# Performance work log

Measured on AMD Instinct MI355X. Metric: run time of the kernel, lower is better.

Reference implementation:

```python
import jax, jax.numpy as jnp
import numpy as np

DIM = 180
HEADS = 6
NSQ = 12          # num_gs_seed_sqrt
N = NSQ * NSQ     # 144 tokens per window
B = 2048


def _relative_position_index(nsq: int) -> np.ndarray:
    coords = np.stack(np.meshgrid(np.arange(nsq), np.arange(nsq), indexing='ij'))  # [2,nsq,nsq]
    flat = coords.reshape(2, -1)                       # [2, N]
    rel = flat[:, :, None] - flat[:, None, :]          # [2, N, N]
    rel = rel.transpose(1, 2, 0)                       # [N, N, 2]
    rel[:, :, 0] += nsq - 1
    rel[:, :, 1] += nsq - 1
    rel[:, :, 0] *= 2 * nsq - 1
    return rel.sum(-1)                                 # [N, N] int

REL_IDX = jnp.asarray(_relative_position_index(NSQ))


def setup_inputs() -> dict:
    key = jax.random.key(0)
    ks = jax.random.split(key, 10)
    d = DIM
    std_lin = 1.0 / np.sqrt(d)
    inp = {
        'gs': jax.random.normal(ks[0], (B, N, d), dtype=jnp.float32),
        'wq': jax.random.normal(ks[1], (d, d), dtype=jnp.float32) * std_lin,
        'bq': jnp.zeros((d,), jnp.float32),
        'wk': jax.random.normal(ks[2], (d, d), dtype=jnp.float32) * std_lin,
        'bk': jnp.zeros((d,), jnp.float32),
        'wv': jax.random.normal(ks[3], (d, d), dtype=jnp.float32) * std_lin,
        'bv': jnp.zeros((d,), jnp.float32),
        'wp': jax.random.normal(ks[4], (d, d), dtype=jnp.float32) * std_lin,
        'bp': jnp.zeros((d,), jnp.float32),
        # trunc_normal(std=0.02) table: [(2*nsq-1)^2, heads]
        'bias_table': jax.random.normal(ks[5], ((2 * NSQ - 1) ** 2, HEADS), dtype=jnp.float32) * 0.02,
    }
    return inp


def reference(gs, wq, bq, wk, bk, wv, bv, wp, bp, bias_table):
    b, n, c = gs.shape
    h = HEADS
    hd = c // h
    scale = hd ** -0.5

    def heads(x, w, bias):
        y = x @ w + bias                                  # [b, n, c]
        return y.reshape(b, n, h, hd).transpose(0, 2, 1, 3)  # [b, h, n, hd]

    q = heads(gs, wq, bq) * scale
    k = heads(gs, wk, bk)
    v = heads(gs, wv, bv)

    attn = jnp.einsum('bhqd,bhkd->bhqk', q, k)            # [b, h, n, n]
    rel_bias = bias_table[REL_IDX]                        # [n, n, h]
    attn = attn + rel_bias.transpose(2, 0, 1)[None]       # + [1, h, n, n]
    attn = jax.nn.softmax(attn, axis=-1)

    out = jnp.einsum('bhqk,bhkd->bhqd', attn, v)          # [b, h, n, hd]
    out = out.transpose(0, 2, 1, 3).reshape(b, n, c)
    return out @ wp + bp
```

## Files before the change

### kernel.cpp

```cpp
#include <hip/hip_runtime.h>


typedef __bf16 bf16_t;
typedef __bf16 bf16x8 __attribute__((ext_vector_type(8)));
typedef __bf16 bf16x4 __attribute__((ext_vector_type(4)));
typedef float f32x4 __attribute__((ext_vector_type(4)));

#define MFMA16(a, b, c) __builtin_amdgcn_mfma_f32_16x16x32_bf16((a), (b), (c), 0, 0, 0)
#define GLDS16(g, l) __builtin_amdgcn_global_load_lds(                         \
    (const __attribute__((address_space(1))) void*)(g),                        \
    (__attribute__((address_space(3))) void*)(l), 16, 0, 0)

static __device__ __forceinline__ f32x4 fzero4() {
    f32x4 z; z[0] = 0.f; z[1] = 0.f; z[2] = 0.f; z[3] = 0.f; return z;
}
static __device__ __forceinline__ bf16x8 bzero8() {
    bf16x8 z;
    #pragma unroll
    for (int i = 0; i < 8; ++i) z[i] = (bf16_t)0.f;
    return z;
}

__global__ void pack_kernel(const float* __restrict__ wq, const float* __restrict__ bq,
                            const float* __restrict__ wk, const float* __restrict__ bk,
                            const float* __restrict__ wv, const float* __restrict__ bv,
                            const float* __restrict__ wp, const float* __restrict__ bt,
                            bf16_t* __restrict__ Wqkv, bf16_t* __restrict__ Wp,
                            bf16_t* __restrict__ BIASf, float* __restrict__ bqkv)
{
    const int t = blockIdx.x * blockDim.x + threadIdx.x;
    const int stride = gridDim.x * blockDim.x;
    const float L2E = 1.4426950408889634f;
    const float qscale = 0.18257418583505536f * L2E;

    for (int i = t; i < 6 * 6 * 6 * 512; i += stride) {
        int j = i & 7, lane = (i >> 3) & 63;
        int f = i >> 9;
        int nt = f % 6, kt = (f / 6) % 6, h = f / 36;
        int kin = kt * 32 + (lane >> 4) * 8 + j;
        int c = nt * 16 + (lane & 15);
        int sec = c >> 5, d = c & 31;
        float v = 0.f;
        if (kin < 180 && d < 30) {
            int col = h * 30 + d;
            if (sec == 0)      v = wq[kin * 180 + col] * qscale;
            else if (sec == 1) v = wk[kin * 180 + col];
            else               v = wv[kin * 180 + col];
        }
        Wqkv[i] = (bf16_t)v;
    }
    for (int i = t; i < 2 * 6 * 6 * 512; i += stride) {
        int j = i & 7, lane = (i >> 3) & 63;
        int f = i >> 9;
        int ntl = f % 6, kt = (f / 6) % 6, half = f / 36;
        int nt = half * 6 + ntl;
        int kin = kt * 32 + (lane >> 4) * 8 + j;
        int hh = kin >> 5, d = kin & 31;
        int cout = nt * 16 + (lane & 15);
        float v = 0.f;
        if (d < 30 && cout < 180) v = wp[(hh * 30 + d) * 180 + cout];
        Wp[i] = (bf16_t)v;
    }
    for (int i = t; i < 6 * 9 * 9 * 64; i += stride) {
        int lane = i & 63;
        int f = i >> 6;
        int nt = f % 9, wvq = (f / 9) % 9, h = f / 81;
        int q = wvq * 16 + (lane & 15);
        int qi = q / 12, qj = q % 12;
        #pragma unroll
        for (int r = 0; r < 4; ++r) {
            int k = nt * 16 + (lane >> 4) * 4 + r;
            int ki = k / 12, kj = k % 12;
            int rel = (qi - ki + 11) * 23 + (qj - kj + 11);
            BIASf[i * 4 + r] = (bf16_t)(bt[rel * 6 + h] * L2E);
        }
    }
    for (int i = t; i < 576; i += stride) {
        int c = i % 96, h = i / 96;
        int sec = c >> 5, d = c & 31;
        float v = 0.f;
        if (d < 30) {
            if (sec == 0)      v = bq[h * 30 + d] * qscale;
            else if (sec == 1) v = bk[h * 30 + d];
            else               v = bv[h * 30 + d];
        }
        bqkv[i] = v;
    }
}

__global__ __launch_bounds__(576, 2)
void attn_kernel(const float* __restrict__ gs,
                 const bf16_t* __restrict__ Wqkv, const bf16_t* __restrict__ Wp,
                 const bf16_t* __restrict__ BIASf, const float* __restrict__ bqkv,
                 const float* __restrict__ bp, float* __restrict__ out)
{
    __shared__ __align__(16) unsigned char smem[152064];

    const int tid = threadIdx.x;
    const int lane = tid & 63;
    const int wv = tid >> 6;
    const int l15 = lane & 15;
    const int lg = lane >> 4;
    const int win = blockIdx.x;
    const float* __restrict__ gsw = gs + (size_t)win * 25920;

    constexpr int WB0     = 0;
    constexpr int WB1     = 36864;
    constexpr int ST_BASE = 73728;
    constexpr int K_BASE  = 115200;
    constexpr int VT_BASE = 133632;

    #pragma unroll
    for (int i = 0; i < 4; ++i) {
        const int base = wv * 64 + i * 576;
        GLDS16((const char*)Wqkv + (size_t)(base + lane) * 16, smem + WB0 + base * 16);
    }
    #pragma unroll
    for (int i = 0; i < 4; ++i) {
        const int base = wv * 64 + i * 576;
        GLDS16((const char*)Wqkv + 36864 + (size_t)(base + lane) * 16, smem + WB1 + base * 16);
    }

    bf16x8 xa[6];
    {
        const int row = wv * 16 + l15;
        const float4* __restrict__ g4 = (const float4*)(gsw + row * 180);
        #pragma unroll
        for (int kt = 0; kt < 6; ++kt) {
            const int c0 = kt * 32 + lg * 8;
            float4 lo = {0.f, 0.f, 0.f, 0.f}, hi = {0.f, 0.f, 0.f, 0.f};
            if (c0 + 4 <= 180) lo = g4[c0 >> 2];
            if (c0 + 8 <= 180) hi = g4[(c0 >> 2) + 1];
            bf16x8 v;
            v[0] = (bf16_t)lo.x; v[1] = (bf16_t)lo.y; v[2] = (bf16_t)lo.z; v[3] = (bf16_t)lo.w;
            v[4] = (bf16_t)hi.x; v[5] = (bf16_t)hi.y; v[6] = (bf16_t)hi.z; v[7] = (bf16_t)hi.w;
            xa[kt] = v;
        }
    }
    __syncthreads();

    bf16x8 ao[6];
    char* const pb = (char*)smem + ST_BASE + wv * 4608;
    const int pswz = (l15 & 6) << 3;
    const int row0 = wv * 16 + lg * 4;

    auto qkv_scatter = [&](const int hh, const int wbofs, bf16_t* q8o) {
        const int KB = K_BASE + (hh & 1) * 9216;
        const int VB = VT_BASE + (hh & 1) * 9216;
        f32x4 acc[6];
        #pragma unroll
        for (int nt = 0; nt < 6; ++nt) acc[nt] = fzero4();
        __builtin_amdgcn_s_setprio(1);
        #pragma unroll
        for (int kt = 0; kt < 6; ++kt) {
            #pragma unroll
            for (int nt = 0; nt < 6; ++nt) {
                bf16x8 bw = *(const bf16x8*)(smem + wbofs + ((kt * 6 + nt) * 64 + lane) * 16);
                acc[nt] = MFMA16(xa[kt], bw, acc[nt]);
            }
        }
        __builtin_amdgcn_s_setprio(0);
        #pragma unroll
        for (int nt = 0; nt < 2; ++nt) {
            const float bias = bqkv[hh * 96 + nt * 16 + l15];
            #pragma unroll
            for (int r = 0; r < 4; ++r)
                q8o[nt * 4 + r] = (bf16_t)(acc[nt][r] + bias);
        }
        #pragma unroll
        for (int nt = 2; nt < 4; ++nt) {
            const float bias = bqkv[hh * 96 + nt * 16 + l15];
            const int d32 = ((nt & 1) << 4) + l15;
            #pragma unroll
            for (int r = 0; r < 4; ++r) {
                const int rr = row0 + r;
                *(bf16_t*)(smem + KB + rr * 64 + ((d32 * 2) ^ ((rr & 6) << 3))) =
                    (bf16_t)(acc[nt][r] + bias);
            }
        }
        #pragma unroll
        for (int nt = 4; nt < 6; ++nt) {
            const float bias = bqkv[hh * 96 + nt * 16 + l15];
            const int d32 = ((nt & 1) << 4) + l15;
            const int vswz = (wv < 8) ? (((d32 >> 2) & 3) << 4) : 0;
            bf16x4 vvv;
            #pragma unroll
            for (int r = 0; r < 4; ++r)
                vvv[r] = (bf16_t)(acc[nt][r] + bias);
            *(bf16x4*)(smem + VB + d32 * 288 + ((row0 * 2) ^ vswz)) = vvv;
        }
    };

    #pragma unroll
    for (int i3 = 0; i3 < 3; ++i3) {
        const int h0 = i3 * 2, h1 = h0 + 1;

        bf16_t q8a[8], q8b[8];
        qkv_scatter(h0, WB0, q8a);
        qkv_scatter(h1, WB1, q8b);
        __syncthreads();

        {
            const char* __restrict__ n0 = (i3 < 2)
                ? ((const char*)Wqkv + (size_t)(h0 + 2) * 36864) : (const char*)Wp;
            const char* __restrict__ n1 = (i3 < 2)
                ? ((const char*)Wqkv + (size_t)(h1 + 2) * 36864) : ((const char*)Wp + 36864);
            #pragma unroll
            for (int i = 0; i < 4; ++i) {
                const int base = wv * 64 + i * 576;
                GLDS16(n0 + (size_t)(base + lane) * 16, smem + WB0 + base * 16);
            }
            #pragma unroll
            for (int i = 0; i < 4; ++i) {
                const int base = wv * 64 + i * 576;
                GLDS16(n1 + (size_t)(base + lane) * 16, smem + WB1 + base * 16);
            }
        }

        #pragma unroll
        for (int r = 0; r < 4; ++r) {
            const int row = lg * 4 + r;
            const int swz = (row & 6) << 3;
            *(bf16_t*)(pb + row * 64 + ((l15 * 2) ^ swz))             = q8a[r];
            *(bf16_t*)(pb + row * 64 + ((l15 * 2 + 32) ^ swz))        = q8a[4 + r];
            *(bf16_t*)(pb + 1024 + row * 64 + ((l15 * 2) ^ swz))      = q8b[r];
            *(bf16_t*)(pb + 1024 + row * 64 + ((l15 * 2 + 32) ^ swz)) = q8b[4 + r];
        }
        asm volatile("" ::: "memory");
        bf16x8 aq0 = *(const bf16x8*)(pb + l15 * 64 + ((lg * 16) ^ ((l15 & 6) << 3)));
        bf16x8 aq1 = *(const bf16x8*)(pb + 1024 + l15 * 64 + ((lg * 16) ^ ((l15 & 6) << 3)));
        asm volatile("" ::: "memory");

        float sum0 = 0.f, sum1 = 0.f;
        f32x4 s1[9];
        #pragma unroll
        for (int nt = 0; nt < 9; ++nt) {
            const int krow = nt * 16 + l15;
            const int ksw = (lg * 16) ^ ((krow & 6) << 3);
            bf16x8 kf0 = *(const bf16x8*)(smem + K_BASE + krow * 64 + ksw);
            bf16x8 kf1 = *(const bf16x8*)(smem + K_BASE + 9216 + krow * 64 + ksw);
            f32x4 sv0 = MFMA16(kf0, aq0, fzero4());
            f32x4 sv1 = MFMA16(kf1, aq1, fzero4());
            bf16x4 b40 = *(const bf16x4*)(BIASf +
                         (size_t)((((h0 * 9 + wv) * 9 + nt) * 64 + lane) * 4));
            bf16x4 b41 = *(const bf16x4*)(BIASf +
                         (size_t)((((h1 * 9 + wv) * 9 + nt) * 64 + lane) * 4));
            bf16x4 pw;
            #pragma unroll
            for (int r = 0; r < 4; ++r) {
                float p = exp2f(sv0[r] + (float)b40[r]);
                sum0 += p;
                pw[r] = (bf16_t)p;
                float q = exp2f(sv1[r] + (float)b41[r]);
                sum1 += q;
                s1[nt][r] = q;
            }
            if (nt < 8)
                *(bf16x4*)(pb + (nt >> 1) * 1024 + l15 * 64 +
                           ((((nt & 1) << 5) + lg * 8) ^ pswz)) = pw;
            else
                *(bf16x4*)(pb + 4096 + l15 * 32 + lg * 8) = pw;
        }
        sum0 += __shfl_xor(sum0, 16, 64);
        sum0 += __shfl_xor(sum0, 32, 64);
        sum1 += __shfl_xor(sum1, 16, 64);
        sum1 += __shfl_xor(sum1, 32, 64);
        const float rinv0 = 1.f / sum0;
        const float rinv1 = 1.f / sum1;
        asm volatile("" ::: "memory");

        f32x4 o00 = fzero4(), o01 = fzero4();
        __builtin_amdgcn_s_setprio(1);
        #pragma unroll
        for (int kt = 0; kt < 4; ++kt) {
            const int vs0 = ((l15 >> 2) & 3) << 4;
            bf16x8 ap  = *(const bf16x8*)(pb + kt * 1024 + l15 * 64 + ((lg * 16) ^ pswz));
            bf16x8 bv0 = *(const bf16x8*)(smem + VT_BASE + l15 * 288 + kt * 64 + ((lg * 16) ^ vs0));
            bf16x8 bv1 = *(const bf16x8*)(smem + VT_BASE + (16 + l15) * 288 + kt * 64 + ((lg * 16) ^ vs0));
            o00 = MFMA16(ap, bv0, o00);
            o01 = MFMA16(ap, bv1, o01);
        }
        {
            bf16x8 ap = bzero8(), bv0 = bzero8(), bv1 = bzero8();
            if (lg < 2) {
                ap  = *(const bf16x8*)(pb + 4096 + l15 * 32 + lg * 16);
                bv0 = *(const bf16x8*)(smem + VT_BASE + l15 * 288 + 256 + lg * 16);
                bv1 = *(const bf16x8*)(smem + VT_BASE + (16 + l15) * 288 + 256 + lg * 16);
            }
            o00 = MFMA16(ap, bv0, o00);
            o01 = MFMA16(ap, bv1, o01);
        }
        __builtin_amdgcn_s_setprio(0);
        asm volatile("" ::: "memory");

        #pragma unroll
        for (int nt = 0; nt < 9; ++nt) {
            bf16x4 pw;
            #pragma unroll
            for (int r = 0; r < 4; ++r) pw[r] = (bf16_t)s1[nt][r];
            if (nt < 8)
                *(bf16x4*)(pb + (nt >> 1) * 1024 + l15 * 64 +
                           ((((nt & 1) << 5) + lg * 8) ^ pswz)) = pw;
            else
                *(bf16x4*)(pb + 4096 + l15 * 32 + lg * 8) = pw;
        }
        asm volatile("" ::: "memory");

        f32x4 o10 = fzero4(), o11 = fzero4();
        __builtin_amdgcn_s_setprio(1);
        #pragma unroll
        for (int kt = 0; kt < 4; ++kt) {
            const int vs0 = ((l15 >> 2) & 3) << 4;
            bf16x8 ap  = *(const bf16x8*)(pb + kt * 1024 + l15 * 64 + ((lg * 16) ^ pswz));
            bf16x8 bv0 = *(const bf16x8*)(smem + VT_BASE + 9216 + l15 * 288 + kt * 64 + ((lg * 16) ^ vs0));
            bf16x8 bv1 = *(const bf16x8*)(smem + VT_BASE + 9216 + (16 + l15) * 288 + kt * 64 + ((lg * 16) ^ vs0));
            o10 = MFMA16(ap, bv0, o10);
            o11 = MFMA16(ap, bv1, o11);
        }
        {
            bf16x8 ap = bzero8(), bv0 = bzero8(), bv1 = bzero8();
            if (lg < 2) {
                ap  = *(const bf16x8*)(pb + 4096 + l15 * 32 + lg * 16);
                bv0 = *(const bf16x8*)(smem + VT_BASE + 9216 + l15 * 288 + 256 + lg * 16);
                bv1 = *(const bf16x8*)(smem + VT_BASE + 9216 + (16 + l15) * 288 + 256 + lg * 16);
            }
            o10 = MFMA16(ap, bv0, o10);
            o11 = MFMA16(ap, bv1, o11);
        }
        __builtin_amdgcn_s_setprio(0);
        asm volatile("" ::: "memory");

        #pragma unroll
        for (int r = 0; r < 4; ++r) {
            const float rq0 = __shfl(rinv0, lg * 4 + r, 16);
            const float rq1 = __shfl(rinv1, lg * 4 + r, 16);
            const int row = lg * 4 + r;
            const int swz = (row & 6) << 3;
            *(bf16_t*)(pb + row * 64 + ((l15 * 2) ^ swz))             = (bf16_t)(o00[r] * rq0);
            *(bf16_t*)(pb + row * 64 + ((l15 * 2 + 32) ^ swz))        = (bf16_t)(o01[r] * rq0);
            *(bf16_t*)(pb + 1024 + row * 64 + ((l15 * 2) ^ swz))      = (bf16_t)(o10[r] * rq1);
            *(bf16_t*)(pb + 1024 + row * 64 + ((l15 * 2 + 32) ^ swz)) = (bf16_t)(o11[r] * rq1);
        }
        asm volatile("" ::: "memory");
        ao[h0] = *(const bf16x8*)(pb + l15 * 64 + ((lg * 16) ^ ((l15 & 6) << 3)));
        ao[h1] = *(const bf16x8*)(pb + 1024 + l15 * 64 + ((lg * 16) ^ ((l15 & 6) << 3)));

        __syncthreads();
    }

    float* __restrict__ og = out + (size_t)win * 25920;
    #pragma unroll
    for (int half = 0; half < 2; ++half) {
        const int WH = half ? WB1 : WB0;
        f32x4 accp[6];
        #pragma unroll
        for (int nt = 0; nt < 6; ++nt) accp[nt] = fzero4();
        __builtin_amdgcn_s_setprio(1);
        #pragma unroll
        for (int kt = 0; kt < 6; ++kt) {
            #pragma unroll
            for (int nt = 0; nt < 6; ++nt) {
                bf16x8 bw = *(const bf16x8*)(smem + WH + ((kt * 6 + nt) * 64 + lane) * 16);
                accp[nt] = MFMA16(ao[kt], bw, accp[nt]);
            }
        }
        __builtin_amdgcn_s_setprio(0);
        #pragma unroll
        for (int nt = 0; nt < 6; ++nt) {
            const int col = half * 96 + nt * 16 + l15;
            if (col < 180) {
                const float bias = bp[col];
                #pragma unroll
                for (int r = 0; r < 4; ++r) {
                    const int row = wv * 16 + lg * 4 + r;
                    og[row * 180 + col] = accp[nt][r] + bias;
                }
            }
        }
    }
}

extern "C" void kernel_launch(void* const* d_in, const int* in_sizes, int n_in,
                              void* d_out, int out_size, void* d_ws, size_t ws_size,
                              hipStream_t stream) {
    const float* gs = (const float*)d_in[0];
    const float* wq = (const float*)d_in[1];
    const float* bq = (const float*)d_in[2];
    const float* wk = (const float*)d_in[3];
    const float* bk = (const float*)d_in[4];
    const float* wv = (const float*)d_in[5];
    const float* bv = (const float*)d_in[6];
    const float* wp = (const float*)d_in[7];
    const float* bp = (const float*)d_in[8];
    const float* bt = (const float*)d_in[9];

    char* ws = (char*)d_ws;
    bf16_t* Wqkv  = (bf16_t*)(ws);
    bf16_t* Wp    = (bf16_t*)(ws + 221184);
    bf16_t* BIASf = (bf16_t*)(ws + 294912);
    float*  bqkv  = (float*)(ws + 543744);

    pack_kernel<<<256, 256, 0, stream>>>(wq, bq, wk, bk, wv, bv, wp, bt,
                                         Wqkv, Wp, BIASf, bqkv);
    attn_kernel<<<2048, 576, 0, stream>>>(gs, Wqkv, Wp, BIASf, bqkv, bp, (float*)d_out);
}
```

Measured before the change: 325.2 us.

## Feed softmax probabilities directly into 16x16x16 MFMA, skipping LDS staging

The P·V product now uses the K=16 bf16 MFMA so the exp'd score registers can serve directly as the A operand, removing the round trip of P through per-wave LDS scratch and the second pass that stored head1's probabilities. Both heads' PV accumulation is interleaved into the score loop, and the scratch region shrinks, cutting LDS allocation per block. This trades twice as many smaller MFMAs and narrower V loads for fewer LDS writes and reads. An inline-asm fallback with s_nop padding is used if the builtin is missing.

```diff
diff --git a/kernel.cpp b/kernel.cpp
--- a/kernel.cpp
+++ b/kernel.cpp
@@ -4,6 +4,7 @@
 typedef __bf16 bf16_t;
 typedef __bf16 bf16x8 __attribute__((ext_vector_type(8)));
 typedef __bf16 bf16x4 __attribute__((ext_vector_type(4)));
+typedef short s16x4 __attribute__((ext_vector_type(4)));
 typedef float f32x4 __attribute__((ext_vector_type(4)));
 
 #define MFMA16(a, b, c) __builtin_amdgcn_mfma_f32_16x16x32_bf16((a), (b), (c), 0, 0, 0)
@@ -11,14 +12,25 @@
     (const __attribute__((address_space(1))) void*)(g),                        \
     (__attribute__((address_space(3))) void*)(l), 16, 0, 0)
 
+static __device__ __forceinline__ s16x4 b2s(bf16x4 v) {
+    s16x4 r; __builtin_memcpy(&r, &v, 8); return r;
+}
+#if __has_builtin(__builtin_amdgcn_mfma_f32_16x16x16bf16_1k)
+static __device__ __forceinline__ f32x4 mfma_k16(bf16x4 a, bf16x4 b, f32x4 c) {
+    return __builtin_amdgcn_mfma_f32_16x16x16bf16_1k(b2s(a), b2s(b), c, 0, 0, 0);
+}
+#define K16_ASM 0
+#else
+static __device__ __forceinline__ f32x4 mfma_k16(bf16x4 a, bf16x4 b, f32x4 c) {
+    asm volatile("v_mfma_f32_16x16x16_bf16 %0, %1, %2, %0"
+                 : "+v"(c) : "v"(a), "v"(b));
+    return c;
+}
+#define K16_ASM 1
+#endif
+
 static __device__ __forceinline__ f32x4 fzero4() {
     f32x4 z; z[0] = 0.f; z[1] = 0.f; z[2] = 0.f; z[3] = 0.f; return z;
-}
-static __device__ __forceinline__ bf16x8 bzero8() {
-    bf16x8 z;
-    #pragma unroll
-    for (int i = 0; i < 8; ++i) z[i] = (bf16_t)0.f;
-    return z;
 }
 
 __global__ void pack_kernel(const float* __restrict__ wq, const float* __restrict__ bq,
@@ -94,7 +106,7 @@
                  const bf16_t* __restrict__ BIASf, const float* __restrict__ bqkv,
                  const float* __restrict__ bp, float* __restrict__ out)
 {
-    __shared__ __align__(16) unsigned char smem[152064];
+    __shared__ __align__(16) unsigned char smem[129024];
 
     const int tid = threadIdx.x;
     const int lane = tid & 63;
@@ -107,8 +119,8 @@
     constexpr int WB0     = 0;
     constexpr int WB1     = 36864;
     constexpr int ST_BASE = 73728;
-    constexpr int K_BASE  = 115200;
-    constexpr int VT_BASE = 133632;
+    constexpr int K_BASE  = 92160;
+    constexpr int VT_BASE = 110592;
 
     #pragma unroll
     for (int i = 0; i < 4; ++i) {
@@ -140,8 +152,7 @@
     __syncthreads();
 
     bf16x8 ao[6];
-    char* const pb = (char*)smem + ST_BASE + wv * 4608;
-    const int pswz = (l15 & 6) << 3;
+    char* const pb = (char*)smem + ST_BASE + wv * 2048;
     const int row0 = wv * 16 + lg * 4;
 
     auto qkv_scatter = [&](const int hh, const int wbofs, bf16_t* q8o) {
@@ -232,7 +243,7 @@
         asm volatile("" ::: "memory");
 
         float sum0 = 0.f, sum1 = 0.f;
-        f32x4 s1[9];
+        f32x4 o00 = fzero4(), o01 = fzero4(), o10 = fzero4(), o11 = fzero4();
         #pragma unroll
         for (int nt = 0; nt < 9; ++nt) {
             const int krow = nt * 16 + l15;
@@ -245,91 +256,38 @@
                          (size_t)((((h0 * 9 + wv) * 9 + nt) * 64 + lane) * 4));
             bf16x4 b41 = *(const bf16x4*)(BIASf +
                          (size_t)((((h1 * 9 + wv) * 9 + nt) * 64 + lane) * 4));
-            bf16x4 pw;
+            bf16x4 p0, p1;
             #pragma unroll
             for (int r = 0; r < 4; ++r) {
-                float p = exp2f(sv0[r] + (float)b40[r]);
-                sum0 += p;
-                pw[r] = (bf16_t)p;
-                float q = exp2f(sv1[r] + (float)b41[r]);
-                sum1 += q;
-                s1[nt][r] = q;
-            }
-            if (nt < 8)
-                *(bf16x4*)(pb + (nt >> 1) * 1024 + l15 * 64 +
-                           ((((nt & 1) << 5) + lg * 8) ^ pswz)) = pw;
-            else
-                *(bf16x4*)(pb + 4096 + l15 * 32 + lg * 8) = pw;
-        }
+                float e0 = exp2f(sv0[r] + (float)b40[r]);
+                sum0 += e0;
+                p0[r] = (bf16_t)e0;
+                float e1 = exp2f(sv1[r] + (float)b41[r]);
+                sum1 += e1;
+                p1[r] = (bf16_t)e1;
+            }
+            const int vtoff = nt * 32 + lg * 8;
+            const int vsw = (nt < 8) ? (((l15 >> 2) & 3) << 4) : 0;
+            bf16x4 v00 = *(const bf16x4*)(smem + VT_BASE + l15 * 288 + (vtoff ^ vsw));
+            bf16x4 v01 = *(const bf16x4*)(smem + VT_BASE + (16 + l15) * 288 + (vtoff ^ vsw));
+            bf16x4 v10 = *(const bf16x4*)(smem + VT_BASE + 9216 + l15 * 288 + (vtoff ^ vsw));
+            bf16x4 v11 = *(const bf16x4*)(smem + VT_BASE + 9216 + (16 + l15) * 288 + (vtoff ^ vsw));
+            o00 = mfma_k16(p0, v00, o00);
+            o01 = mfma_k16(p0, v01, o01);
+            o10 = mfma_k16(p1, v10, o10);
+            o11 = mfma_k16(p1, v11, o11);
+        }
+#if K16_ASM
+        asm volatile("s_nop 7\n\ts_nop 7");
+#endif
         sum0 += __shfl_xor(sum0, 16, 64);
         sum0 += __shfl_xor(sum0, 32, 64);
         sum1 += __shfl_xor(sum1, 16, 64);
         sum1 += __shfl_xor(sum1, 32, 64);
         const float rinv0 = 1.f / sum0;
         const float rinv1 = 1.f / sum1;
+
         asm volatile("" ::: "memory");
-
-        f32x4 o00 = fzero4(), o01 = fzero4();
-        __builtin_amdgcn_s_setprio(1);
-        #pragma unroll
-        for (int kt = 0; kt < 4; ++kt) {
-            const int vs0 = ((l15 >> 2) & 3) << 4;
-            bf16x8 ap  = *(const bf16x8*)(pb + kt * 1024 + l15 * 64 + ((lg * 16) ^ pswz));
-            bf16x8 bv0 = *(const bf16x8*)(smem + VT_BASE + l15 * 288 + kt * 64 + ((lg * 16) ^ vs0));
-            bf16x8 bv1 = *(const bf16x8*)(smem + VT_BASE + (16 + l15) * 288 + kt * 64 + ((lg * 16) ^ vs0));
-            o00 = MFMA16(ap, bv0, o00);
-            o01 = MFMA16(ap, bv1, o01);
-        }
-        {
-            bf16x8 ap = bzero8(), bv0 = bzero8(), bv1 = bzero8();
-            if (lg < 2) {
-                ap  = *(const bf16x8*)(pb + 4096 + l15 * 32 + lg * 16);
-                bv0 = *(const bf16x8*)(smem + VT_BASE + l15 * 288 + 256 + lg * 16);
-                bv1 = *(const bf16x8*)(smem + VT_BASE + (16 + l15) * 288 + 256 + lg * 16);
-            }
-            o00 = MFMA16(ap, bv0, o00);
-            o01 = MFMA16(ap, bv1, o01);
-        }
-        __builtin_amdgcn_s_setprio(0);
-        asm volatile("" ::: "memory");
-
-        #pragma unroll
-        for (int nt = 0; nt < 9; ++nt) {
-            bf16x4 pw;
-            #pragma unroll
-            for (int r = 0; r < 4; ++r) pw[r] = (bf16_t)s1[nt][r];
-            if (nt < 8)
-                *(bf16x4*)(pb + (nt >> 1) * 1024 + l15 * 64 +
-                           ((((nt & 1) << 5) + lg * 8) ^ pswz)) = pw;
-            else
-                *(bf16x4*)(pb + 4096 + l15 * 32 + lg * 8) = pw;
-        }
-        asm volatile("" ::: "memory");
-
-        f32x4 o10 = fzero4(), o11 = fzero4();
-        __builtin_amdgcn_s_setprio(1);
-        #pragma unroll
-        for (int kt = 0; kt < 4; ++kt) {
-            const int vs0 = ((l15 >> 2) & 3) << 4;
-            bf16x8 ap  = *(const bf16x8*)(pb + kt * 1024 + l15 * 64 + ((lg * 16) ^ pswz));
-            bf16x8 bv0 = *(const bf16x8*)(smem + VT_BASE + 9216 + l15 * 288 + kt * 64 + ((lg * 16) ^ vs0));
-            bf16x8 bv1 = *(const bf16x8*)(smem + VT_BASE + 9216 + (16 + l15) * 288 + kt * 64 + ((lg * 16) ^ vs0));
-            o10 = MFMA16(ap, bv0, o10);
-            o11 = MFMA16(ap, bv1, o11);
-        }
-        {
-            bf16x8 ap = bzero8(), bv0 = bzero8(), bv1 = bzero8();
-            if (lg < 2) {
-                ap  = *(const bf16x8*)(pb + 4096 + l15 * 32 + lg * 16);
-                bv0 = *(const bf16x8*)(smem + VT_BASE + 9216 + l15 * 288 + 256 + lg * 16);
-                bv1 = *(const bf16x8*)(smem + VT_BASE + 9216 + (16 + l15) * 288 + 256 + lg * 16);
-            }
-            o10 = MFMA16(ap, bv0, o10);
-            o11 = MFMA16(ap, bv1, o11);
-        }
-        __builtin_amdgcn_s_setprio(0);
-        asm volatile("" ::: "memory");
-
         #pragma unroll
         for (int r = 0; r < 4; ++r) {
             const float rq0 = __shfl(rinv0, lg * 4 + r, 16);
```

New measurement: 408.8 us. 25.7% more time.
